# Kernel optimization log

Hardware: AMD Instinct MI355X
Metric: run time of the kernel (lower is better)

## Reference

```python
import jax, jax.numpy as jnp
import numpy as np


def butterfly_mult(twiddle, x):
    # twiddle: (S, M, n//2, 2, 2); x: (B, S, n); increasing_stride=True
    B, S, n = x.shape
    M = twiddle.shape[1]
    out = x
    for idx in range(M):  # loop over log2(n) stages (structural, not data dim)
        stride = 1 << idx
        g = n // (2 * stride)
        t = twiddle[:, idx].reshape(S, g, stride, 2, 2)   # (S, g, r, i, j)
        xr = out.reshape(B, S, g, 2, stride)              # (B, S, g, j, r)
        out = jnp.einsum('sgrij,bsgjr->bsgir', t, xr).reshape(B, S, n)
    return out


def butterfly_layer(x, twiddle, bias, out_size):
    # x: (..., n) with n a power of 2 (pre_process pad is a no-op)
    lead = x.shape[:-1]
    n = x.shape[-1]
    S = twiddle.shape[0]
    xb = x.reshape(-1, n)
    xb = jnp.broadcast_to(xb[:, None, :], (xb.shape[0], S, n))  # expand to nstacks
    out = butterfly_mult(twiddle, xb)
    out = out.reshape(out.shape[0], S * n)[:, :out_size] + bias[:out_size]
    return out.reshape(*lead, out_size)


def setup_inputs() -> dict:
    key = jax.random.key(0)
    ks = jax.random.split(key, 5)
    B, T, D, H = 4, 4096, 1024, 4096
    inv_sqrt2 = 1.0 / np.sqrt(2.0).astype(np.float32)
    x = jax.random.normal(ks[0], (B, T, D), jnp.float32)
    tw1 = jax.random.normal(ks[1], (4, 10, 512, 2, 2), jnp.float32) * inv_sqrt2
    b1 = jax.random.normal(ks[2], (H,), jnp.float32) * 0.02
    tw2 = jax.random.normal(ks[3], (1, 11, 1024, 2, 2), jnp.float32) * inv_sqrt2
    b2 = jax.random.normal(ks[4], (D,), jnp.float32) * 0.02
    return {"x": x, "tw1": tw1, "b1": b1, "tw2": tw2, "b2": b2}


def reference(x, tw1, b1, tw2, b2):
    # GLU: fc1 (butterfly) -> chunk -> x * sigmoid(gates) -> fc2 (butterfly)
    h = butterfly_layer(x, tw1, b1, 4096)      # (B, T, 4096)
    a, gates = jnp.split(h, 2, axis=-1)        # (B, T, 2048) each
    h = a * jax.nn.sigmoid(gates)
    return butterfly_layer(h, tw2, b2, 1024)   # (B, T, 1024)
```

## Files before the change

kernel.cpp:

```cpp
#include <hip/hip_runtime.h>
#include <cstdint>


#define NTHR 512
#define NBLK 2048

typedef float        v4f __attribute__((ext_vector_type(4)));
typedef unsigned int u4i __attribute__((ext_vector_type(4)));

struct F8 { v4f lo, hi; };

__device__ __forceinline__ float sigmf(float g) {
    return __builtin_amdgcn_rcpf(1.0f + __expf(-g));
}

__device__ __forceinline__ v4f sig4(v4f g) {
    v4f r;
    r.x = sigmf(g.x); r.y = sigmf(g.y); r.z = sigmf(g.z); r.w = sigmf(g.w);
    return r;
}

__device__ __forceinline__ int swz(int e) { return e ^ ((e >> 4) & 7); }

__device__ __forceinline__ unsigned pk2(float a, float b) {
    unsigned ua = __float_as_uint(a) + 0x8000u;
    unsigned ub = __float_as_uint(b) + 0x8000u;
    return __builtin_amdgcn_perm(ub, ua, 0x07060302u);
}

__device__ __forceinline__ u4i packF8(const F8& v) {
    u4i r;
    r.x = pk2(v.lo.x, v.lo.y);
    r.y = pk2(v.lo.z, v.lo.w);
    r.z = pk2(v.hi.x, v.hi.y);
    r.w = pk2(v.hi.z, v.hi.w);
    return r;
}

__device__ __forceinline__ F8 unpackF8(u4i u) {
    F8 v;
    v.lo.x = __uint_as_float(u.x << 16);
    v.lo.y = __uint_as_float(u.x & 0xffff0000u);
    v.lo.z = __uint_as_float(u.y << 16);
    v.lo.w = __uint_as_float(u.y & 0xffff0000u);
    v.hi.x = __uint_as_float(u.z << 16);
    v.hi.y = __uint_as_float(u.z & 0xffff0000u);
    v.hi.z = __uint_as_float(u.w << 16);
    v.hi.w = __uint_as_float(u.w & 0xffff0000u);
    return v;
}

__device__ __forceinline__ void bfly(F8& a, F8& b, const v4f t) {
    v4f n0l = t.x * a.lo + t.y * b.lo;
    v4f n0h = t.x * a.hi + t.y * b.hi;
    v4f n1l = t.z * a.lo + t.w * b.lo;
    v4f n1h = t.z * a.hi + t.w * b.hi;
    a.lo = n0l; a.hi = n0h; b.lo = n1l; b.hi = n1h;
}

template<int K>
__device__ __forceinline__ void l2pass(u4i* lds, const v4f* tw2q, int t) {
    const int low   = t & ((1 << K) - 1);
    const int hi    = t >> K;
    const int pbase = low | (hi << (K + 2));
    F8 v[4];
    #pragma unroll
    for (int r = 0; r < 4; ++r) v[r] = unpackF8(lds[swz(pbase | (r << K))]);
    {
        const v4f* tq = tw2q + K * 1024 + (low | (hi << (K + 1)));
        bfly(v[0], v[1], tq[0]);
        bfly(v[2], v[3], tq[1 << K]);
    }
    {
        const v4f* tq = tw2q + (K + 1) * 1024 + (low | (hi << (K + 1)));
        bfly(v[0], v[2], tq[0]);
        bfly(v[1], v[3], tq[1 << K]);
    }
    #pragma unroll
    for (int r = 0; r < 4; ++r) lds[swz(pbase | (r << K))] = packF8(v[r]);
}

__global__ __launch_bounds__(NTHR, 4) void glu_butterfly(
    const float* __restrict__ x, const float* __restrict__ tw1,
    const float* __restrict__ b1, const float* __restrict__ tw2,
    const float* __restrict__ b2, float* __restrict__ out)
{
    extern __shared__ u4i lds[];
    const int t    = threadIdx.x;
    const int row0 = blockIdx.x * 8;
    const v4f* tw1q = (const v4f*)tw1;
    const v4f* tw2q = (const v4f*)tw2;

    {
        const int s = t >> 7;
        const int c = t & 127;
        float xs[8][8];
        const float* xb = x + (size_t)row0 * 1024 + c * 8;
        #pragma unroll
        for (int rr = 0; rr < 8; ++rr) {
            const v4f* xp = (const v4f*)(xb + rr * 1024);
            v4f a = xp[0], b = xp[1];
            xs[rr][0] = a.x; xs[rr][1] = a.y; xs[rr][2] = a.z; xs[rr][3] = a.w;
            xs[rr][4] = b.x; xs[rr][5] = b.y; xs[rr][6] = b.z; xs[rr][7] = b.w;
        }
        F8 d[8];
        #pragma unroll
        for (int k = 0; k < 8; ++k) {
            d[k].lo = (v4f){xs[0][k], xs[1][k], xs[2][k], xs[3][k]};
            d[k].hi = (v4f){xs[4][k], xs[5][k], xs[6][k], xs[7][k]};
        }
        #pragma unroll
        for (int j = 0; j < 3; ++j) {
            const v4f* tq = tw1q + (s * 10 + j) * 512 + c * 4;
            #pragma unroll
            for (int m = 0; m < 4; ++m) {
                const int i0 = ((m >> j) << (j + 1)) | (m & ((1 << j) - 1));
                bfly(d[i0], d[i0 | (1 << j)], tq[m]);
            }
        }
        const int ebase = s * 1024 + c * 8;
        #pragma unroll
        for (int k = 0; k < 8; ++k) lds[swz(ebase + k)] = packF8(d[k]);
    }
    __syncthreads();

    {
        const int low = t & 7, hi = t >> 3;
        const int s = hi >> 4;
        const int pbase = low | (hi << 6);
        F8 v[8];
        #pragma unroll
        for (int r = 0; r < 8; ++r) v[r] = unpackF8(lds[swz(pbase | (r << 3))]);
        #pragma unroll
        for (int jj = 0; jj < 3; ++jj) {
            const v4f* tq = tw1q + (s * 10 + 3 + jj) * 512 + (low | ((hi & 15) << 5));
            #pragma unroll
            for (int m = 0; m < 4; ++m) {
                const int r0 = ((m >> jj) << (jj + 1)) | (m & ((1 << jj) - 1));
                bfly(v[r0], v[r0 | (1 << jj)], tq[m << 3]);
            }
        }
        #pragma unroll
        for (int r = 0; r < 8; ++r) lds[swz(pbase | (r << 3))] = packF8(v[r]);
    }
    __syncthreads();

    {
        const int low = t & 63, hi = t >> 6;
        const int s = hi >> 1;
        const int pbase = low | (hi << 9);
        F8 v[8];
        #pragma unroll
        for (int r = 0; r < 8; ++r) v[r] = unpackF8(lds[swz(pbase | (r << 6))]);
        #pragma unroll
        for (int jj = 0; jj < 3; ++jj) {
            const v4f* tq = tw1q + (s * 10 + 6 + jj) * 512 + (low | ((hi & 1) << 8));
            #pragma unroll
            for (int m = 0; m < 4; ++m) {
                const int r0 = ((m >> jj) << (jj + 1)) | (m & ((1 << jj) - 1));
                bfly(v[r0], v[r0 | (1 << jj)], tq[m << 6]);
            }
        }
        #pragma unroll
        for (int r = 0; r < 8; ++r) lds[swz(pbase | (r << 6))] = packF8(v[r]);
    }
    __syncthreads();

    {
        const int t8 = t & 255, th = t >> 8;
        F8 d[8];
        #pragma unroll
        for (int c = 0; c < 2; ++c)
        #pragma unroll
        for (int b = 0; b < 2; ++b)
        #pragma unroll
        for (int a = 0; a < 2; ++a) {
            const int e = (t8 << 1) | a | (b << 9) | (th << 10) | (c << 11);
            d[(c << 2) | (b << 1) | a] = unpackF8(lds[swz(e)]);
        }
        #pragma unroll
        for (int c = 0; c < 2; ++c)
        #pragma unroll
        for (int a = 0; a < 2; ++a) {
            const v4f tw9 = tw1q[((th | (c << 1)) * 10 + 9) * 512 + ((t8 << 1) | a)];
            bfly(d[(c << 2) | a], d[(c << 2) | 2 | a], tw9);
        }
        #pragma unroll
        for (int c = 0; c < 2; ++c)
        #pragma unroll
        for (int b = 0; b < 2; ++b)
        #pragma unroll
        for (int a = 0; a < 2; ++a) {
            const float bb = b1[(th | (c << 1)) * 1024 + ((t8 << 1) | a | (b << 9))];
            F8& dv = d[(c << 2) | (b << 1) | a];
            dv.lo += bb; dv.hi += bb;
        }
        F8 u[4];
        #pragma unroll
        for (int i = 0; i < 4; ++i) {
            u[i].lo = d[i].lo * sig4(d[4 | i].lo);
            u[i].hi = d[i].hi * sig4(d[4 | i].hi);
        }
        #pragma unroll
        for (int b = 0; b < 2; ++b) {
            const v4f tw0 = tw2q[t8 | (b << 8) | (th << 9)];
            bfly(u[b << 1], u[(b << 1) | 1], tw0);
        }
        #pragma unroll
        for (int b = 0; b < 2; ++b)
        #pragma unroll
        for (int a = 0; a < 2; ++a) {
            const int e = (t8 << 1) | a | (b << 9) | (th << 10);
            lds[swz(e)] = packF8(u[(b << 1) | a]);
        }
    }
    __syncthreads();

    l2pass<1>(lds, tw2q, t); __syncthreads();
    l2pass<3>(lds, tw2q, t); __syncthreads();
    l2pass<5>(lds, tw2q, t); __syncthreads();
    l2pass<7>(lds, tw2q, t); __syncthreads();

    {
        F8 v[4];
        #pragma unroll
        for (int r = 0; r < 4; ++r) v[r] = unpackF8(lds[swz(t | (r << 9))]);
        bfly(v[0], v[1], tw2q[9 * 1024 + t]);
        bfly(v[2], v[3], tw2q[9 * 1024 + (t | 512)]);
        bfly(v[0], v[2], tw2q[10 * 1024 + t]);
        bfly(v[1], v[3], tw2q[10 * 1024 + (t | 512)]);
        #pragma unroll
        for (int r = 0; r < 2; ++r) {
            const int p = t | (r << 9);
            const float bb = b2[p];
            float* ob = out + (size_t)row0 * 1024 + p;
            ob[0*1024] = v[r].lo.x + bb;
            ob[1*1024] = v[r].lo.y + bb;
            ob[2*1024] = v[r].lo.z + bb;
            ob[3*1024] = v[r].lo.w + bb;
            ob[4*1024] = v[r].hi.x + bb;
            ob[5*1024] = v[r].hi.y + bb;
            ob[6*1024] = v[r].hi.z + bb;
            ob[7*1024] = v[r].hi.w + bb;
        }
    }
}

extern "C" void kernel_launch(void* const* d_in, const int* in_sizes, int n_in,
                              void* d_out, int out_size, void* d_ws, size_t ws_size,
                              hipStream_t stream) {
    const float* x   = (const float*)d_in[0];
    const float* tw1 = (const float*)d_in[1];
    const float* b1  = (const float*)d_in[2];
    const float* tw2 = (const float*)d_in[3];
    const float* b2  = (const float*)d_in[4];
    float* outp = (float*)d_out;

    (void)hipFuncSetAttribute((const void*)glu_butterfly,
                              hipFuncAttributeMaxDynamicSharedMemorySize, 65536);
    glu_butterfly<<<NBLK, NTHR, 65536, stream>>>(x, tw1, b1, tw2, b2, outp);
}
```

Before: 187.6 us.

## Recast butterfly stages as 32x32 block matrices computed on bf16 MFMA

A pre-kernel multiplies out each group of five butterfly stages into dense 32x32 bf16 block matrices and writes them to workspace. The main kernel then runs both butterfly layers as bf16 MFMA matrix multiplies, staging data through swizzled LDS and fusing the GLU gating and biases. It processes 32 rows per block instead of 8. This swaps many scalar FMA passes and LDS barriers for tensor-core work, at the cost of more total FLOPs, a large LDS footprint that limits occupancy, and extra bf16 rounding of the combined matrices.

After: 172.3 us. 8.1% less time.

```diff
diff --git a/kernel.cpp b/kernel.cpp
--- a/kernel.cpp
+++ b/kernel.cpp
@@ -2,25 +2,12 @@
 #include <cstdint>
 
 
-#define NTHR 512
-#define NBLK 2048
-
-typedef float        v4f __attribute__((ext_vector_type(4)));
-typedef unsigned int u4i __attribute__((ext_vector_type(4)));
-
-struct F8 { v4f lo, hi; };
-
-__device__ __forceinline__ float sigmf(float g) {
-    return __builtin_amdgcn_rcpf(1.0f + __expf(-g));
-}
-
-__device__ __forceinline__ v4f sig4(v4f g) {
-    v4f r;
-    r.x = sigmf(g.x); r.y = sigmf(g.y); r.z = sigmf(g.z); r.w = sigmf(g.w);
-    return r;
-}
-
-__device__ __forceinline__ int swz(int e) { return e ^ ((e >> 4) & 7); }
+typedef float          v4f __attribute__((ext_vector_type(4)));
+typedef unsigned int   u4i __attribute__((ext_vector_type(4)));
+typedef unsigned int   u2i __attribute__((ext_vector_type(2)));
+typedef short          bf8 __attribute__((ext_vector_type(8)));
+
+#define MFMA16(A, B, C) __builtin_amdgcn_mfma_f32_16x16x32_bf16(A, B, C, 0, 0, 0)
 
 __device__ __forceinline__ unsigned pk2(float a, float b) {
     unsigned ua = __float_as_uint(a) + 0x8000u;
@@ -28,221 +15,278 @@
     return __builtin_amdgcn_perm(ub, ua, 0x07060302u);
 }
 
-__device__ __forceinline__ u4i packF8(const F8& v) {
-    u4i r;
-    r.x = pk2(v.lo.x, v.lo.y);
-    r.y = pk2(v.lo.z, v.lo.w);
-    r.z = pk2(v.hi.x, v.hi.y);
-    r.w = pk2(v.hi.z, v.hi.w);
+__device__ __forceinline__ float sigmf(float g) {
+    return __builtin_amdgcn_rcpf(1.0f + __expf(-g));
+}
+__device__ __forceinline__ v4f sig4(v4f g) {
+    v4f r; r.x = sigmf(g.x); r.y = sigmf(g.y); r.z = sigmf(g.z); r.w = sigmf(g.w);
     return r;
 }
 
-__device__ __forceinline__ F8 unpackF8(u4i u) {
-    F8 v;
-    v.lo.x = __uint_as_float(u.x << 16);
-    v.lo.y = __uint_as_float(u.x & 0xffff0000u);
-    v.lo.z = __uint_as_float(u.y << 16);
-    v.lo.w = __uint_as_float(u.y & 0xffff0000u);
-    v.hi.x = __uint_as_float(u.z << 16);
-    v.hi.y = __uint_as_float(u.z & 0xffff0000u);
-    v.hi.z = __uint_as_float(u.w << 16);
-    v.hi.w = __uint_as_float(u.w & 0xffff0000u);
-    return v;
-}
-
-__device__ __forceinline__ void bfly(F8& a, F8& b, const v4f t) {
-    v4f n0l = t.x * a.lo + t.y * b.lo;
-    v4f n0h = t.x * a.hi + t.y * b.hi;
-    v4f n1l = t.z * a.lo + t.w * b.lo;
-    v4f n1h = t.z * a.hi + t.w * b.hi;
-    a.lo = n0l; a.hi = n0h; b.lo = n1l; b.hi = n1h;
-}
-
-template<int K>
-__device__ __forceinline__ void l2pass(u4i* lds, const v4f* tw2q, int t) {
-    const int low   = t & ((1 << K) - 1);
-    const int hi    = t >> K;
-    const int pbase = low | (hi << (K + 2));
-    F8 v[4];
-    #pragma unroll
-    for (int r = 0; r < 4; ++r) v[r] = unpackF8(lds[swz(pbase | (r << K))]);
+__device__ __forceinline__ int ab(int row, int hw) {
+    return (row << 11) + (((hw) << 1) ^ ((row & 7) << 4));
+}
+
+__global__ void build_mats(const float* __restrict__ tw1,
+                           const float* __restrict__ tw2,
+                           unsigned short* __restrict__ wsm)
+{
+    const int mid = blockIdx.x * 2 + (threadIdx.x >> 5);
+    const int c   = threadIdx.x & 31;
+
+    const float* twf; int np, rbase, rstep, j0, scaleb = -1, l2s = 0;
+    if (mid < 128)      { twf = tw1 + (mid >> 5) * 20480;        np = 512;  rbase = (mid & 31) * 32; rstep = 1;  j0 = 0; }
+    else if (mid < 256) { twf = tw1 + ((mid - 128) >> 5) * 20480; np = 512; rbase = mid & 31;        rstep = 32; j0 = 5; }
+    else if (mid < 320) { twf = tw2; np = 1024; rbase = (mid - 256) * 32; rstep = 1; j0 = 0; }
+    else                { twf = tw2; np = 1024; l2s = mid & 31; scaleb = (mid - 320) >> 5;
+                          rbase = l2s + (scaleb << 10); rstep = 32; j0 = 5; }
+
+    float v[32];
+    #pragma unroll
+    for (int r = 0; r < 32; ++r) v[r] = (r == c) ? 1.0f : 0.0f;
+
+    #pragma unroll
+    for (int jj = 0; jj < 5; ++jj) {
+        const int j = j0 + jj;
+        #pragma unroll
+        for (int pr = 0; pr < 16; ++pr) {
+            const int r0   = ((pr >> jj) << (jj + 1)) | (pr & ((1 << jj) - 1));
+            const int r1   = r0 | (1 << jj);
+            const int p0   = rbase + r0 * rstep;
+            const int tidx = ((p0 >> (j + 1)) << j) | (p0 & ((1 << j) - 1));
+            const v4f T    = *(const v4f*)(twf + (size_t)(j * np + tidx) * 4);
+            const float a = v[r0], b = v[r1];
+            v[r0] = T.x * a + T.y * b;
+            v[r1] = T.z * a + T.w * b;
+        }
+    }
+    if (scaleb >= 0) {
+        #pragma unroll
+        for (int r = 0; r < 32; ++r)
+            v[r] *= tw2[(size_t)(10 * 1024 + l2s + 32 * r) * 4 + scaleb];
+    }
+    #pragma unroll
+    for (int r = 0; r < 32; ++r) {
+        const int mt   = r >> 4;
+        const int lane = (r & 15) + ((c >> 3) << 4);
+        wsm[((size_t)(mid * 2 + mt) * 64 + lane) * 8 + (c & 7)] =
+            (unsigned short)((__float_as_uint(v[r]) + 0x8000u) >> 16);
+    }
+}
+
+__global__ __launch_bounds__(512) void glu_bfly(
+    const float* __restrict__ x, const float* __restrict__ b1,
+    const float* __restrict__ b2, const bf8* __restrict__ mats,
+    float* __restrict__ out)
+{
+    extern __shared__ char lds[];
+    char*  actA = lds;
+    char*  actB = lds + 65536;
+    float* b1t  = (float*)(lds + 131072);
+
+    const int t = threadIdx.x, w = t >> 6, l = t & 63, lr = l & 15, lk = l >> 4;
+    const int row0 = blockIdx.x * 32;
+    const v4f vz = {0.f, 0.f, 0.f, 0.f};
+
     {
-        const v4f* tq = tw2q + K * 1024 + (low | (hi << (K + 1)));
-        bfly(v[0], v[1], tq[0]);
-        bfly(v[2], v[3], tq[1 << K]);
-    }
-    {
-        const v4f* tq = tw2q + (K + 1) * 1024 + (low | (hi << (K + 1)));
-        bfly(v[0], v[2], tq[0]);
-        bfly(v[1], v[3], tq[1 << K]);
-    }
-    #pragma unroll
-    for (int r = 0; r < 4; ++r) lds[swz(pbase | (r << K))] = packF8(v[r]);
-}
-
-__global__ __launch_bounds__(NTHR, 4) void glu_butterfly(
-    const float* __restrict__ x, const float* __restrict__ tw1,
-    const float* __restrict__ b1, const float* __restrict__ tw2,
-    const float* __restrict__ b2, float* __restrict__ out)
-{
-    extern __shared__ u4i lds[];
-    const int t    = threadIdx.x;
-    const int row0 = blockIdx.x * 8;
-    const v4f* tw1q = (const v4f*)tw1;
-    const v4f* tw2q = (const v4f*)tw2;
-
-    {
-        const int s = t >> 7;
-        const int c = t & 127;
-        float xs[8][8];
-        const float* xb = x + (size_t)row0 * 1024 + c * 8;
-        #pragma unroll
-        for (int rr = 0; rr < 8; ++rr) {
-            const v4f* xp = (const v4f*)(xb + rr * 1024);
-            v4f a = xp[0], b = xp[1];
-            xs[rr][0] = a.x; xs[rr][1] = a.y; xs[rr][2] = a.z; xs[rr][3] = a.w;
-            xs[rr][4] = b.x; xs[rr][5] = b.y; xs[rr][6] = b.z; xs[rr][7] = b.w;
-        }
-        F8 d[8];
+        const v4f* bp = (const v4f*)(b1 + t * 8);
+        const v4f a = bp[0], b = bp[1];
+        const float vals[8] = {a.x, a.y, a.z, a.w, b.x, b.y, b.z, b.w};
         #pragma unroll
         for (int k = 0; k < 8; ++k) {
-            d[k].lo = (v4f){xs[0][k], xs[1][k], xs[2][k], xs[3][k]};
-            d[k].hi = (v4f){xs[4][k], xs[5][k], xs[6][k], xs[7][k]};
-        }
-        #pragma unroll
-        for (int j = 0; j < 3; ++j) {
-            const v4f* tq = tw1q + (s * 10 + j) * 512 + c * 4;
-            #pragma unroll
-            for (int m = 0; m < 4; ++m) {
-                const int i0 = ((m >> j) << (j + 1)) | (m & ((1 << j) - 1));
-                bfly(d[i0], d[i0 | (1 << j)], tq[m]);
-            }
-        }
-        const int ebase = s * 1024 + c * 8;
-        #pragma unroll
-        for (int k = 0; k < 8; ++k) lds[swz(ebase + k)] = packF8(d[k]);
+            const int gid = t * 8 + k, s = gid >> 10, r = gid & 1023;
+            b1t[(s << 10) + ((r & 31) << 5) + (r >> 5)] = vals[k];
+        }
+    }
+
+    bf8 xf[4][2];
+    #pragma unroll
+    for (int gi = 0; gi < 4; ++gi)
+    #pragma unroll
+    for (int nh = 0; nh < 2; ++nh) {
+        const float* xp = x + (size_t)(row0 + nh * 16 + lr) * 1024 + (w * 4 + gi) * 32 + lk * 8;
+        const v4f a = *(const v4f*)xp;
+        const v4f b = *(const v4f*)(xp + 4);
+        u4i uu; uu.x = pk2(a.x, a.y); uu.y = pk2(a.z, a.w);
+        uu.z = pk2(b.x, b.y); uu.w = pk2(b.z, b.w);
+        xf[gi][nh] = __builtin_bit_cast(bf8, uu);
     }
     __syncthreads();
 
-    {
-        const int low = t & 7, hi = t >> 3;
-        const int s = hi >> 4;
-        const int pbase = low | (hi << 6);
-        F8 v[8];
-        #pragma unroll
-        for (int r = 0; r < 8; ++r) v[r] = unpackF8(lds[swz(pbase | (r << 3))]);
-        #pragma unroll
-        for (int jj = 0; jj < 3; ++jj) {
-            const v4f* tq = tw1q + (s * 10 + 3 + jj) * 512 + (low | ((hi & 15) << 5));
-            #pragma unroll
-            for (int m = 0; m < 4; ++m) {
-                const int r0 = ((m >> jj) << (jj + 1)) | (m & ((1 << jj) - 1));
-                bfly(v[r0], v[r0 | (1 << jj)], tq[m << 3]);
-            }
-        }
-        #pragma unroll
-        for (int r = 0; r < 8; ++r) lds[swz(pbase | (r << 3))] = packF8(v[r]);
-    }
-    __syncthreads();
-
-    {
-        const int low = t & 63, hi = t >> 6;
-        const int s = hi >> 1;
-        const int pbase = low | (hi << 9);
-        F8 v[8];
-        #pragma unroll
-        for (int r = 0; r < 8; ++r) v[r] = unpackF8(lds[swz(pbase | (r << 6))]);
-        #pragma unroll
-        for (int jj = 0; jj < 3; ++jj) {
-            const v4f* tq = tw1q + (s * 10 + 6 + jj) * 512 + (low | ((hi & 1) << 8));
-            #pragma unroll
-            for (int m = 0; m < 4; ++m) {
-                const int r0 = ((m >> jj) << (jj + 1)) | (m & ((1 << jj) - 1));
-                bfly(v[r0], v[r0 | (1 << jj)], tq[m << 6]);
-            }
-        }
-        #pragma unroll
-        for (int r = 0; r < 8; ++r) lds[swz(pbase | (r << 6))] = packF8(v[r]);
-    }
-    __syncthreads();
-
-    {
-        const int t8 = t & 255, th = t >> 8;
-        F8 d[8];
-        #pragma unroll
-        for (int c = 0; c < 2; ++c)
-        #pragma unroll
-        for (int b = 0; b < 2; ++b)
-        #pragma unroll
-        for (int a = 0; a < 2; ++a) {
-            const int e = (t8 << 1) | a | (b << 9) | (th << 10) | (c << 11);
-            d[(c << 2) | (b << 1) | a] = unpackF8(lds[swz(e)]);
-        }
-        #pragma unroll
-        for (int c = 0; c < 2; ++c)
-        #pragma unroll
-        for (int a = 0; a < 2; ++a) {
-            const v4f tw9 = tw1q[((th | (c << 1)) * 10 + 9) * 512 + ((t8 << 1) | a)];
-            bfly(d[(c << 2) | a], d[(c << 2) | 2 | a], tw9);
-        }
-        #pragma unroll
-        for (int c = 0; c < 2; ++c)
-        #pragma unroll
-        for (int b = 0; b < 2; ++b)
-        #pragma unroll
-        for (int a = 0; a < 2; ++a) {
-            const float bb = b1[(th | (c << 1)) * 1024 + ((t8 << 1) | a | (b << 9))];
-            F8& dv = d[(c << 2) | (b << 1) | a];
-            dv.lo += bb; dv.hi += bb;
-        }
-        F8 u[4];
-        #pragma unroll
-        for (int i = 0; i < 4; ++i) {
-            u[i].lo = d[i].lo * sig4(d[4 | i].lo);
-            u[i].hi = d[i].hi * sig4(d[4 | i].hi);
-        }
-        #pragma unroll
-        for (int b = 0; b < 2; ++b) {
-            const v4f tw0 = tw2q[t8 | (b << 8) | (th << 9)];
-            bfly(u[b << 1], u[(b << 1) | 1], tw0);
-        }
-        #pragma unroll
-        for (int b = 0; b < 2; ++b)
-        #pragma unroll
-        for (int a = 0; a < 2; ++a) {
-            const int e = (t8 << 1) | a | (b << 9) | (th << 10);
-            lds[swz(e)] = packF8(u[(b << 1) | a]);
-        }
-    }
-    __syncthreads();
-
-    l2pass<1>(lds, tw2q, t); __syncthreads();
-    l2pass<3>(lds, tw2q, t); __syncthreads();
-    l2pass<5>(lds, tw2q, t); __syncthreads();
-    l2pass<7>(lds, tw2q, t); __syncthreads();
-
-    {
-        F8 v[4];
-        #pragma unroll
-        for (int r = 0; r < 4; ++r) v[r] = unpackF8(lds[swz(t | (r << 9))]);
-        bfly(v[0], v[1], tw2q[9 * 1024 + t]);
-        bfly(v[2], v[3], tw2q[9 * 1024 + (t | 512)]);
-        bfly(v[0], v[2], tw2q[10 * 1024 + t]);
-        bfly(v[1], v[3], tw2q[10 * 1024 + (t | 512)]);
-        #pragma unroll
-        for (int r = 0; r < 2; ++r) {
-            const int p = t | (r << 9);
-            const float bb = b2[p];
-            float* ob = out + (size_t)row0 * 1024 + p;
-            ob[0*1024] = v[r].lo.x + bb;
-            ob[1*1024] = v[r].lo.y + bb;
-            ob[2*1024] = v[r].lo.z + bb;
-            ob[3*1024] = v[r].lo.w + bb;
-            ob[4*1024] = v[r].hi.x + bb;
-            ob[5*1024] = v[r].hi.y + bb;
-            ob[6*1024] = v[r].hi.z + bb;
-            ob[7*1024] = v[r].hi.w + bb;
-        }
+    unsigned z0p[4][2][2][2];
+    v4f fin[4][2][2];
+
+    #pragma unroll
+    for (int h = 0; h < 2; ++h) {
+        const int sa = h, sg = h + 2;
+
+        #pragma unroll
+        for (int pass = 0; pass < 2; ++pass) {
+            const int s = (pass == 0) ? sa : sg;
+            char* dst = (pass == 0) ? actA : actB;
+            v4f acc[4][2][2];
+            #pragma unroll
+            for (int gi = 0; gi < 4; ++gi) {
+                const int mid = s * 32 + w * 4 + gi;
+                const bf8 a0 = mats[(mid * 2 + 0) * 64 + l];
+                const bf8 a1 = mats[(mid * 2 + 1) * 64 + l];
+                #pragma unroll
+                for (int nh = 0; nh < 2; ++nh) {
+                    acc[gi][nh][0] = MFMA16(a0, xf[gi][nh], vz);
+                    acc[gi][nh][1] = MFMA16(a1, xf[gi][nh], vz);
+                }
+            }
+            #pragma unroll
+            for (int nh = 0; nh < 2; ++nh)
+            #pragma unroll
+            for (int mt = 0; mt < 2; ++mt)
+            #pragma unroll
+            for (int rg = 0; rg < 4; ++rg) {
+                const int m = mt * 16 + lk * 4 + rg;
+                u2i pv;
+                pv.x = pk2(acc[0][nh][mt][rg], acc[1][nh][mt][rg]);
+                pv.y = pk2(acc[2][nh][mt][rg], acc[3][nh][mt][rg]);
+                *(u2i*)(dst + ab(nh * 16 + lr, 32 * m + 4 * w)) = pv;
+            }
+            __syncthreads();
+        }
+
+        {
+            v4f uacc[4][2][2];
+            #pragma unroll
+            for (int li = 0; li < 4; ++li) {
+                const int lg = w * 4 + li;
+                v4f ha[2][2], hg[2][2];
+                {
+                    const int mid = 128 + sa * 32 + lg;
+                    const bf8 a0 = mats[(mid * 2 + 0) * 64 + l];
+                    const bf8 a1 = mats[(mid * 2 + 1) * 64 + l];
+                    const bf8 f0 = *(const bf8*)(actA + ab(lr,      32 * lg + 8 * lk));
+                    const bf8 f1 = *(const bf8*)(actA + ab(16 + lr, 32 * lg + 8 * lk));
+                    ha[0][0] = MFMA16(a0, f0, vz); ha[0][1] = MFMA16(a1, f0, vz);
+                    ha[1][0] = MFMA16(a0, f1, vz); ha[1][1] = MFMA16(a1, f1, vz);
+                }
+                {
+                    const int mid = 128 + sg * 32 + lg;
+                    const bf8 a0 = mats[(mid * 2 + 0) * 64 + l];
+                    const bf8 a1 = mats[(mid * 2 + 1) * 64 + l];
+                    const bf8 f0 = *(const bf8*)(actB + ab(lr,      32 * lg + 8 * lk));
+                    const bf8 f1 = *(const bf8*)(actB + ab(16 + lr, 32 * lg + 8 * lk));
+                    hg[0][0] = MFMA16(a0, f0, vz); hg[0][1] = MFMA16(a1, f0, vz);
+                    hg[1][0] = MFMA16(a0, f1, vz); hg[1][1] = MFMA16(a1, f1, vz);
+                }
+                #pragma unroll
+                for (int mt = 0; mt < 2; ++mt) {
+                    const v4f ba = *(const v4f*)&b1t[((sa * 32 + lg) << 5) + mt * 16 + lk * 4];
+                    const v4f bg = *(const v4f*)&b1t[((sg * 32 + lg) << 5) + mt * 16 + lk * 4];
+                    #pragma unroll
+                    for (int nh = 0; nh < 2; ++nh)
+                        uacc[li][nh][mt] = (ha[nh][mt] + ba) * sig4(hg[nh][mt] + bg);
+                }
+            }
+            __syncthreads();
+            #pragma unroll
+            for (int nh = 0; nh < 2; ++nh)
+            #pragma unroll
+            for (int mt = 0; mt < 2; ++mt)
+            #pragma unroll
+            for (int rg = 0; rg < 4; ++rg) {
+                const int m = mt * 16 + lk * 4 + rg;
+                u2i pv;
+                pv.x = pk2(uacc[0][nh][mt][rg], uacc[1][nh][mt][rg]);
+                pv.y = pk2(uacc[2][nh][mt][rg], uacc[3][nh][mt][rg]);
+                *(u2i*)(actA + ab(nh * 16 + lr, 32 * m + 4 * w)) = pv;
+            }
+            __syncthreads();
+        }
+
+        {
+            v4f acc[4][2][2];
+            #pragma unroll
+            for (int gi = 0; gi < 4; ++gi) {
+                const int g = w * 4 + gi, mid = 256 + 32 * h + g;
+                const bf8 a0 = mats[(mid * 2 + 0) * 64 + l];
+                const bf8 a1 = mats[(mid * 2 + 1) * 64 + l];
+                #pragma unroll
+                for (int nh = 0; nh < 2; ++nh) {
+                    const bf8 f = *(const bf8*)(actA + ab(nh * 16 + lr, 32 * g + 8 * lk));
+                    acc[gi][nh][0] = MFMA16(a0, f, vz);
+                    acc[gi][nh][1] = MFMA16(a1, f, vz);
+                }
+            }
+            #pragma unroll
+            for (int nh = 0; nh < 2; ++nh)
+            #pragma unroll
+            for (int mt = 0; mt < 2; ++mt)
+            #pragma unroll
+            for (int rg = 0; rg < 4; ++rg) {
+                const int m = mt * 16 + lk * 4 + rg;
+                u2i pv;
+                pv.x = pk2(acc[0][nh][mt][rg], acc[1][nh][mt][rg]);
+                pv.y = pk2(acc[2][nh][mt][rg], acc[3][nh][mt][rg]);
+                *(u2i*)(actB + ab(nh * 16 + lr, 32 * m + 4 * w)) = pv;
+            }
+            __syncthreads();
+        }
+
+        #pragma unroll
+        for (int li = 0; li < 4; ++li) {
+            const int lg = w * 4 + li, mid = 320 + 32 * h + lg;
+            const bf8 a0 = mats[(mid * 2 + 0) * 64 + l];
+            const bf8 a1 = mats[(mid * 2 + 1) * 64 + l];
+            const bf8 f0 = *(const bf8*)(actB + ab(lr,      32 * lg + 8 * lk));
+            const bf8 f1 = *(const bf8*)(actB + ab(16 + lr, 32 * lg + 8 * lk));
+            v4f zz[2][2];
+            zz[0][0] = MFMA16(a0, f0, vz); zz[0][1] = MFMA16(a1, f0, vz);
+            zz[1][0] = MFMA16(a0, f1, vz); zz[1][1] = MFMA16(a1, f1, vz);
+            if (h == 0) {
+                #pragma unroll
+                for (int nh = 0; nh < 2; ++nh)
+                #pragma unroll
+                for (int mt = 0; mt < 2; ++mt) {
+                    z0p[li][nh][mt][0] = pk2(zz[nh][mt].x, zz[nh][mt].y);
+                    z0p[li][nh][mt][1] = pk2(zz[nh][mt].z, zz[nh][mt].w);
+                }
+            } else {
+                #pragma unroll
+                for (int nh = 0; nh < 2; ++nh)
+                #pragma unroll
+                for (int mt = 0; mt < 2; ++mt) {
+                    v4f uz;
+                    uz.x = __uint_as_float(z0p[li][nh][mt][0] << 16);
+                    uz.y = __uint_as_float(z0p[li][nh][mt][0] & 0xffff0000u);
+                    uz.z = __uint_as_float(z0p[li][nh][mt][1] << 16);
+                    uz.w = __uint_as_float(z0p[li][nh][mt][1] & 0xffff0000u);
+                    fin[li][nh][mt] = zz[nh][mt] + uz;
+                }
+            }
+        }
+    }
+
+    #pragma unroll
+    for (int nh = 0; nh < 2; ++nh) {
+        #pragma unroll
+        for (int mt = 0; mt < 2; ++mt)
+        #pragma unroll
+        for (int rg = 0; rg < 4; ++rg) {
+            const int p0 = 4 * w + 32 * (mt * 16 + lk * 4 + rg);
+            v4f vv;
+            vv.x = fin[0][nh][mt][rg]; vv.y = fin[1][nh][mt][rg];
+            vv.z = fin[2][nh][mt][rg]; vv.w = fin[3][nh][mt][rg];
+            *(v4f*)(actA + (lr << 12) + ((p0 << 2) ^ ((lr & 7) << 4))) = vv;
+        }
+        __syncthreads();
+        {
+            const int row = t >> 5, c0 = (t & 31) * 4;
+            #pragma unroll
+            for (int i = 0; i < 8; ++i) {
+                const int col = c0 + 128 * i;
+                v4f ov = *(const v4f*)(actA + (row << 12) + ((col << 2) ^ ((row & 7) << 4)));
+                ov += *(const v4f*)(b2 + col);
+                *(v4f*)(out + (size_t)(row0 + nh * 16 + row) * 1024 + col) = ov;
+            }
+        }
+        __syncthreads();
     }
 }
 
@@ -254,9 +298,11 @@
     const float* b1  = (const float*)d_in[2];
     const float* tw2 = (const float*)d_in[3];
     const float* b2  = (const float*)d_in[4];
-    float* outp = (float*)d_out;
-
-    (void)hipFuncSetAttribute((const void*)glu_butterfly,
-                              hipFuncAttributeMaxDynamicSharedMemorySize, 65536);
-    glu_butterfly<<<NBLK, NTHR, 65536, stream>>>(x, tw1, b1, tw2, b2, outp);
-}
+
+    build_mats<<<192, 64, 0, stream>>>(tw1, tw2, (unsigned short*)d_ws);
+
+    (void)hipFuncSetAttribute((const void*)glu_bfly,
+                              hipFuncAttributeMaxDynamicSharedMemorySize, 147456);
+    glu_bfly<<<512, 512, 147456, stream>>>(x, b1, b2, (const bf8*)d_ws,
+                                           (float*)d_out);
+}
```
